# Performance work log

Measured on AMD Instinct MI355X. Metric: run time of the kernel, lower is better.

## Reference

```python
import jax, jax.numpy as jnp
import numpy as np

# Catmull-Rom basis: hermiteBasis @ tangent matrix (uniform spacing, deltas = 1,1,1)
_HERMITE = np.array([[2, -2, 1, 1], [-3, 3, -2, -1], [0, 0, 1, 0], [1, 0, 0, 0]], dtype=np.float32)
_CR = np.array([[0, 1, 0, 0], [0, 0, 1, 0], [-0.5, 0, 0.5, 0], [0, -0.5, 0, 0.5]], dtype=np.float32)
UNIFORM_BASIS = jnp.asarray(_HERMITE @ _CR)  # [[-0.5,1.5,-1.5,0.5],[1,-2.5,2,-0.5],[-0.5,0,0.5,0],[0,1,0,0]]

D, Z, Y, X, C = 16, 64, 128, 128, 2
N = 262144


def setup_inputs() -> dict:
    key = jax.random.key(0)
    k1, k2 = jax.random.split(key)
    u = jax.random.uniform(k1, (N, 3), dtype=jnp.float32)
    # zyx coords in [1, dim-3] so the 4-knot window stays mostly interior
    idx = u * jnp.array([Z - 4, Y - 4, X - 4], dtype=jnp.float32) + 1.0
    knots = jax.random.normal(k2, (D, Z, Y, X, C), dtype=jnp.float32)
    depth = jnp.float32(7.3)  # in (depths[0], depths[-1]) with depths = arange(1, D+1)
    return {"idx": idx, "knots": knots, "depth": depth}


def _spline_idx(coord, size):
    """coord: [N] float. Returns ([N,4] int knot indices, [N,4] spline weights)."""
    i0 = coord.astype(jnp.int32)                      # trunc == floor for positive coords
    s = jnp.clip(coord - i0.astype(coord.dtype), 0.0, 1.0)
    knot_idx = jnp.clip((i0 - 1)[:, None] + jnp.arange(4, dtype=jnp.int32)[None, :], 0, size - 1)
    # powers [s^3, s^2, s, 1] (explicit stack avoids 0**0 grad issues)
    powers = jnp.stack([s * s * s, s * s, s, jnp.ones_like(s)], axis=1)  # [N,4]
    return knot_idx, powers @ UNIFORM_BASIS


def reference(idx, knots, depth):
    D_, Z_, Y_, X_, _ = knots.shape
    n = idx.shape[0]
    depths = jnp.arange(1, D_ + 1, dtype=jnp.float32)  # uniform spacing -> time_diffs all 1
    ind = jnp.searchsorted(depths, depth, side='right')
    r = (depth - depths[ind - 1]) / (depths[ind] - depths[ind - 1])
    depth_coord = jnp.full((n,), (ind - 1).astype(jnp.float32) + r)

    idp, cd = _spline_idx(depth_coord, D_)
    iz, cz = _spline_idx(idx[:, 0], Z_)
    iy, cy = _spline_idx(idx[:, 1], Y_)
    ix, cx = _spline_idx(idx[:, 2], X_)

    # gather [N,4,4,4,4,C] knot neighborhood, then separable weighted reduction
    sel = knots[idp[:, :, None, None, None],
                iz[:, None, :, None, None],
                iy[:, None, None, :, None],
                ix[:, None, None, None, :]]
    return jnp.einsum('ndzyxc,nd,nz,ny,nx->nc', sel, cd, cz, cy, cx)
```

## Files before the change

### kernel.cpp

```cpp
#include <hip/hip_runtime.h>

#define Dd 16
#define Zd 64
#define Yd 128
#define Xd 128
#define Cd 2

__device__ __forceinline__ void spline_w(float coord, int size, int* idx4, float* w) {
    int i0 = (int)coord;
    float s = coord - (float)i0;
    s = fminf(fmaxf(s, 0.0f), 1.0f);
#pragma unroll
    for (int j = 0; j < 4; ++j) {
        int k = i0 - 1 + j;
        idx4[j] = min(max(k, 0), size - 1);
    }
    float s2 = s * s, s3 = s2 * s;
    w[0] = -0.5f * s3 + s2 - 0.5f * s;
    w[1] =  1.5f * s3 - 2.5f * s2 + 1.0f;
    w[2] = -1.5f * s3 + 2.0f * s2 + 0.5f * s;
    w[3] =  0.5f * s3 - 0.5f * s2;
}

__device__ __forceinline__ void depth_w(float depth, int* id4, float* wd) {
    float dc = depth - 1.0f;
    spline_w(dc, Dd, id4, wd);
}

__global__ void depth_contract_kernel(const float* __restrict__ knots,
                                      const float* __restrict__ depth_p,
                                      float4* __restrict__ Wv) {
    const int nv = Zd * Yd * Xd * Cd / 4;
    int t = blockIdx.x * blockDim.x + threadIdx.x;
    if (t >= nv) return;

    int id[4]; float wd[4];
    depth_w(depth_p[0], id, wd);

    const float4* kv = (const float4*)knots;
    const size_t slice = (size_t)Zd * Yd * Xd * Cd / 4;
    float4 a = kv[(size_t)id[0] * slice + t];
    float4 b = kv[(size_t)id[1] * slice + t];
    float4 c = kv[(size_t)id[2] * slice + t];
    float4 d = kv[(size_t)id[3] * slice + t];
    float4 r;
    r.x = wd[0] * a.x + wd[1] * b.x + wd[2] * c.x + wd[3] * d.x;
    r.y = wd[0] * a.y + wd[1] * b.y + wd[2] * c.y + wd[3] * d.y;
    r.z = wd[0] * a.z + wd[1] * b.z + wd[2] * c.z + wd[3] * d.z;
    r.w = wd[0] * a.w + wd[1] * b.w + wd[2] * c.w + wd[3] * d.w;
    Wv[t] = r;
}

__global__ void gather_eval_kernel(const float* __restrict__ idx,
                                   const float* __restrict__ W,
                                   float* __restrict__ out, int n_pts) {
    int t = blockIdx.x * blockDim.x + threadIdx.x;
    int n = t >> 2;
    int q = t & 3;
    if (n >= n_pts) return;

    float zc = idx[n * 3 + 0];
    float yc = idx[n * 3 + 1];
    float xc = idx[n * 3 + 2];

    int iz[4], iy[4], ix[4];
    float wz[4], wy[4], wx[4];
    spline_w(zc, Zd, iz, wz);
    spline_w(yc, Yd, iy, wy);
    spline_w(xc, Xd, ix, wx);

    const int ixq = ix[q];
    const float wxq = wx[q];

    const float2* __restrict__ Wv = (const float2*)W;

    float r0 = 0.0f, r1 = 0.0f;
#pragma unroll
    for (int a = 0; a < 4; ++a) {
        const int zoff = iz[a] * (Yd * Xd);
#pragma unroll
        for (int b = 0; b < 4; ++b) {
            float2 v = Wv[(size_t)(zoff + iy[b] * Xd + ixq)];
            float wzy = wz[a] * wy[b];
            r0 = fmaf(wzy, v.x, r0);
            r1 = fmaf(wzy, v.y, r1);
        }
    }
    r0 *= wxq;
    r1 *= wxq;

    r0 += __shfl_xor(r0, 1);
    r0 += __shfl_xor(r0, 2);
    r1 += __shfl_xor(r1, 1);
    r1 += __shfl_xor(r1, 2);

    if (q == 0) {
        float2* ov = (float2*)out;
        float2 o; o.x = r0; o.y = r1;
        ov[n] = o;
    }
}

__global__ void fused_kernel(const float* __restrict__ idx,
                             const float* __restrict__ knots,
                             const float* __restrict__ depth_p,
                             float* __restrict__ out, int n_pts) {
    int n = blockIdx.x * blockDim.x + threadIdx.x;
    if (n >= n_pts) return;

    int id[4]; float wd[4];
    depth_w(depth_p[0], id, wd);

    float zc = idx[n * 3 + 0];
    float yc = idx[n * 3 + 1];
    float xc = idx[n * 3 + 2];

    int iz[4], iy[4], ix[4];
    float wz[4], wy[4], wx[4];
    spline_w(zc, Zd, iz, wz);
    spline_w(yc, Yd, iy, wy);
    spline_w(xc, Xd, ix, wx);

    float acc0 = 0.0f, acc1 = 0.0f;
    for (int dd = 0; dd < 4; ++dd) {
        const float* base = knots + (size_t)id[dd] * Zd * Yd * Xd * Cd;
        float d0 = 0.0f, d1 = 0.0f;
#pragma unroll
        for (int a = 0; a < 4; ++a) {
#pragma unroll
            for (int b = 0; b < 4; ++b) {
                const float2* row = (const float2*)(base + ((size_t)(iz[a] * Yd + iy[b]) * Xd) * Cd);
                float r0 = 0.0f, r1 = 0.0f;
#pragma unroll
                for (int qq = 0; qq < 4; ++qq) {
                    float2 v = row[ix[qq]];
                    r0 = fmaf(wx[qq], v.x, r0);
                    r1 = fmaf(wx[qq], v.y, r1);
                }
                float wzy = wz[a] * wy[b];
                d0 = fmaf(wzy, r0, d0);
                d1 = fmaf(wzy, r1, d1);
            }
        }
        acc0 = fmaf(wd[dd], d0, acc0);
        acc1 = fmaf(wd[dd], d1, acc1);
    }
    out[n * 2 + 0] = acc0;
    out[n * 2 + 1] = acc1;
}

extern "C" void kernel_launch(void* const* d_in, const int* in_sizes, int n_in,
                              void* d_out, int out_size, void* d_ws, size_t ws_size,
                              hipStream_t stream) {
    const float* idx   = (const float*)d_in[0];
    const float* knots = (const float*)d_in[1];
    const float* depth = (const float*)d_in[2];
    float* out = (float*)d_out;
    const int n_pts = in_sizes[0] / 3;

    const size_t need = (size_t)Zd * Yd * Xd * Cd * sizeof(float);
    if (ws_size >= need) {
        float* W = (float*)d_ws;
        const int nv = Zd * Yd * Xd * Cd / 4;
        depth_contract_kernel<<<(nv + 255) / 256, 256, 0, stream>>>(knots, depth, (float4*)W);
        const int nthreads = n_pts * 4;
        gather_eval_kernel<<<(nthreads + 255) / 256, 256, 0, stream>>>(idx, W, out, n_pts);
    } else {
        fused_kernel<<<(n_pts + 255) / 256, 256, 0, stream>>>(idx, knots, depth, out, n_pts);
    }
}
```

Measured before the change: 213.9 us.

## Bucket-sort points by z/y tile and evaluate from LDS-resident slabs

```diff
diff --git a/kernel.cpp b/kernel.cpp
--- a/kernel.cpp
+++ b/kernel.cpp
@@ -6,6 +6,16 @@
 #define Xd 128
 #define Cd 2
 
+#define NBUCK_Z 31
+#define NBUCK_Y 16
+#define NBUCK (NBUCK_Z * NBUCK_Y)
+#define NBUCK_PAD 512
+
+#define SZ 5
+#define SY 11
+#define XPAD2 134
+#define SLAB_F4 (SZ * SY * 67)
+
 __device__ __forceinline__ void spline_w(float coord, int size, int* idx4, float* w) {
     int i0 = (int)coord;
     float s = coord - (float)i0;
@@ -22,20 +32,24 @@
     w[3] =  0.5f * s3 - 0.5f * s2;
 }
 
-__device__ __forceinline__ void depth_w(float depth, int* id4, float* wd) {
-    float dc = depth - 1.0f;
-    spline_w(dc, Dd, id4, wd);
+__device__ __forceinline__ int bucket_of(float zc, float yc) {
+    int i0z = (int)zc, i0y = (int)yc;
+    int tz = min(max(i0z >> 1, 0), NBUCK_Z - 1);
+    int ty = min(max(i0y >> 3, 0), NBUCK_Y - 1);
+    return tz * NBUCK_Y + ty;
 }
 
 __global__ void depth_contract_kernel(const float* __restrict__ knots,
                                       const float* __restrict__ depth_p,
-                                      float4* __restrict__ Wv) {
+                                      float4* __restrict__ Wv,
+                                      int* __restrict__ counts) {
     const int nv = Zd * Yd * Xd * Cd / 4;
     int t = blockIdx.x * blockDim.x + threadIdx.x;
+    if (t < NBUCK_PAD) counts[t] = 0;
     if (t >= nv) return;
 
     int id[4]; float wd[4];
-    depth_w(depth_p[0], id, wd);
+    spline_w(depth_p[0] - 1.0f, Dd, id, wd);
 
     const float4* kv = (const float4*)knots;
     const size_t slice = (size_t)Zd * Yd * Xd * Cd / 4;
@@ -51,54 +65,133 @@
     Wv[t] = r;
 }
 
+__global__ void hist_kernel(const float* __restrict__ idx, int n_pts,
+                            int* __restrict__ counts) {
+    int n = blockIdx.x * blockDim.x + threadIdx.x;
+    if (n >= n_pts) return;
+    atomicAdd(&counts[bucket_of(idx[n * 3], idx[n * 3 + 1])], 1);
+}
+
+__global__ __launch_bounds__(NBUCK_PAD) void scan_kernel(const int* __restrict__ counts,
+                                                         int* __restrict__ offsets,
+                                                         int* __restrict__ cursors) {
+    __shared__ int tmp[NBUCK_PAD];
+    int t = threadIdx.x;
+    int v = counts[t];
+    tmp[t] = v;
+    __syncthreads();
+    for (int off = 1; off < NBUCK_PAD; off <<= 1) {
+        int x = (t >= off) ? tmp[t - off] : 0;
+        __syncthreads();
+        tmp[t] += x;
+        __syncthreads();
+    }
+    int excl = tmp[t] - v;
+    offsets[t] = excl;
+    cursors[t] = excl;
+}
+
+__global__ void scatter_kernel(const float* __restrict__ idx, int n_pts,
+                               int* __restrict__ cursors,
+                               float4* __restrict__ sorted_pts) {
+    int n = blockIdx.x * blockDim.x + threadIdx.x;
+    if (n >= n_pts) return;
+    float zc = idx[n * 3], yc = idx[n * 3 + 1], xc = idx[n * 3 + 2];
+    int pos = atomicAdd(&cursors[bucket_of(zc, yc)], 1);
+    float4 sp;
+    sp.x = zc; sp.y = yc; sp.z = xc; sp.w = __int_as_float(n);
+    sorted_pts[pos] = sp;
+}
+
+__global__ __launch_bounds__(256) void bucket_eval_kernel(const float4* __restrict__ sorted_pts,
+                                                          const int* __restrict__ offsets,
+                                                          const int* __restrict__ counts,
+                                                          const float* __restrict__ W,
+                                                          float* __restrict__ out) {
+    __shared__ float4 slab4[SLAB_F4];
+    const int b = blockIdx.x;
+    const int tz = b / NBUCK_Y, ty = b - tz * NBUCK_Y;
+    const int zbase = min(max(2 * tz - 1, 0), Zd - SZ);
+    const int ybase = min(max(8 * ty - 1, 0), Yd - SY);
+    const int tid = threadIdx.x;
+
+    const float4* Wv4 = (const float4*)W;
+    for (int i = tid; i < SZ * SY * 64; i += 256) {
+        int r = i >> 6, j = i & 63;
+        int dz = r / SY, dy = r - dz * SY;
+        slab4[r * 67 + j] = Wv4[(size_t)((zbase + dz) * Yd + (ybase + dy)) * 64 + j];
+    }
+    __syncthreads();
+
+    const float2* __restrict__ slab2 = (const float2*)slab4;
+    const int start = offsets[b];
+    const int cnt4 = counts[b] * 4;
+    float2* __restrict__ ov = (float2*)out;
+
+    for (int i = tid; i < cnt4; i += 256) {
+        int p = i >> 2, q = i & 3;
+        float4 sp = sorted_pts[start + p];
+
+        int iz[4], iy[4], ix[4];
+        float wz[4], wy[4], wx[4];
+        spline_w(sp.x, Zd, iz, wz);
+        spline_w(sp.y, Yd, iy, wy);
+        spline_w(sp.z, Xd, ix, wx);
+
+        const int ixq = ix[q];
+        const float wxq = wx[q];
+
+        float r0 = 0.0f, r1 = 0.0f;
+#pragma unroll
+        for (int a = 0; a < 4; ++a) {
+            const int rz = (iz[a] - zbase) * SY;
+#pragma unroll
+            for (int bb = 0; bb < 4; ++bb) {
+                float2 v = slab2[(rz + (iy[bb] - ybase)) * XPAD2 + ixq];
+                float wzy = wz[a] * wy[bb];
+                r0 = fmaf(wzy, v.x, r0);
+                r1 = fmaf(wzy, v.y, r1);
+            }
+        }
+        r0 *= wxq; r1 *= wxq;
+        r0 += __shfl_xor(r0, 1); r0 += __shfl_xor(r0, 2);
+        r1 += __shfl_xor(r1, 1); r1 += __shfl_xor(r1, 2);
+        if (q == 0) {
+            float2 o; o.x = r0; o.y = r1;
+            ov[__float_as_int(sp.w)] = o;
+        }
+    }
+}
+
 __global__ void gather_eval_kernel(const float* __restrict__ idx,
                                    const float* __restrict__ W,
                                    float* __restrict__ out, int n_pts) {
     int t = blockIdx.x * blockDim.x + threadIdx.x;
-    int n = t >> 2;
-    int q = t & 3;
-    if (n >= n_pts) return;
-
-    float zc = idx[n * 3 + 0];
-    float yc = idx[n * 3 + 1];
-    float xc = idx[n * 3 + 2];
-
+    int n = t >> 2, q = t & 3;
+    if (n >= n_pts) return;
     int iz[4], iy[4], ix[4];
     float wz[4], wy[4], wx[4];
-    spline_w(zc, Zd, iz, wz);
-    spline_w(yc, Yd, iy, wy);
-    spline_w(xc, Xd, ix, wx);
-
-    const int ixq = ix[q];
-    const float wxq = wx[q];
-
-    const float2* __restrict__ Wv = (const float2*)W;
-
+    spline_w(idx[n * 3 + 0], Zd, iz, wz);
+    spline_w(idx[n * 3 + 1], Yd, iy, wy);
+    spline_w(idx[n * 3 + 2], Xd, ix, wx);
+    const int ixq = ix[q]; const float wxq = wx[q];
+    const float2* Wv = (const float2*)W;
     float r0 = 0.0f, r1 = 0.0f;
 #pragma unroll
     for (int a = 0; a < 4; ++a) {
         const int zoff = iz[a] * (Yd * Xd);
 #pragma unroll
-        for (int b = 0; b < 4; ++b) {
-            float2 v = Wv[(size_t)(zoff + iy[b] * Xd + ixq)];
-            float wzy = wz[a] * wy[b];
+        for (int bb = 0; bb < 4; ++bb) {
+            float2 v = Wv[(size_t)(zoff + iy[bb] * Xd + ixq)];
+            float wzy = wz[a] * wy[bb];
             r0 = fmaf(wzy, v.x, r0);
             r1 = fmaf(wzy, v.y, r1);
         }
     }
-    r0 *= wxq;
-    r1 *= wxq;
-
-    r0 += __shfl_xor(r0, 1);
-    r0 += __shfl_xor(r0, 2);
-    r1 += __shfl_xor(r1, 1);
-    r1 += __shfl_xor(r1, 2);
-
-    if (q == 0) {
-        float2* ov = (float2*)out;
-        float2 o; o.x = r0; o.y = r1;
-        ov[n] = o;
-    }
+    r0 *= wxq; r1 *= wxq;
+    r0 += __shfl_xor(r0, 1); r0 += __shfl_xor(r0, 2);
+    r1 += __shfl_xor(r1, 1); r1 += __shfl_xor(r1, 2);
+    if (q == 0) { float2 o; o.x = r0; o.y = r1; ((float2*)out)[n] = o; }
 }
 
 __global__ void fused_kernel(const float* __restrict__ idx,
@@ -107,41 +200,30 @@
                              float* __restrict__ out, int n_pts) {
     int n = blockIdx.x * blockDim.x + threadIdx.x;
     if (n >= n_pts) return;
-
     int id[4]; float wd[4];
-    depth_w(depth_p[0], id, wd);
-
-    float zc = idx[n * 3 + 0];
-    float yc = idx[n * 3 + 1];
-    float xc = idx[n * 3 + 2];
-
+    spline_w(depth_p[0] - 1.0f, Dd, id, wd);
     int iz[4], iy[4], ix[4];
     float wz[4], wy[4], wx[4];
-    spline_w(zc, Zd, iz, wz);
-    spline_w(yc, Yd, iy, wy);
-    spline_w(xc, Xd, ix, wx);
-
+    spline_w(idx[n * 3 + 0], Zd, iz, wz);
+    spline_w(idx[n * 3 + 1], Yd, iy, wy);
+    spline_w(idx[n * 3 + 2], Xd, ix, wx);
     float acc0 = 0.0f, acc1 = 0.0f;
     for (int dd = 0; dd < 4; ++dd) {
         const float* base = knots + (size_t)id[dd] * Zd * Yd * Xd * Cd;
         float d0 = 0.0f, d1 = 0.0f;
-#pragma unroll
-        for (int a = 0; a < 4; ++a) {
-#pragma unroll
-            for (int b = 0; b < 4; ++b) {
-                const float2* row = (const float2*)(base + ((size_t)(iz[a] * Yd + iy[b]) * Xd) * Cd);
+        for (int a = 0; a < 4; ++a)
+            for (int bb = 0; bb < 4; ++bb) {
+                const float2* row = (const float2*)(base + ((size_t)(iz[a] * Yd + iy[bb]) * Xd) * Cd);
                 float r0 = 0.0f, r1 = 0.0f;
-#pragma unroll
                 for (int qq = 0; qq < 4; ++qq) {
                     float2 v = row[ix[qq]];
                     r0 = fmaf(wx[qq], v.x, r0);
                     r1 = fmaf(wx[qq], v.y, r1);
                 }
-                float wzy = wz[a] * wy[b];
+                float wzy = wz[a] * wy[bb];
                 d0 = fmaf(wzy, r0, d0);
                 d1 = fmaf(wzy, r1, d1);
             }
-        }
         acc0 = fmaf(wd[dd], d0, acc0);
         acc1 = fmaf(wd[dd], d1, acc1);
     }
@@ -158,13 +240,33 @@
     float* out = (float*)d_out;
     const int n_pts = in_sizes[0] / 3;
 
-    const size_t need = (size_t)Zd * Yd * Xd * Cd * sizeof(float);
+    const size_t wBytes = (size_t)Zd * Yd * Xd * Cd * sizeof(float);
+    const size_t offCounts  = wBytes;
+    const size_t offOffsets = offCounts + NBUCK_PAD * sizeof(int);
+    const size_t offCursors = offOffsets + NBUCK_PAD * sizeof(int);
+    size_t offSorted = offCursors + NBUCK_PAD * sizeof(int);
+    offSorted = (offSorted + 15) & ~(size_t)15;
+    const size_t need = offSorted + (size_t)n_pts * sizeof(float4);
+
+    char* ws = (char*)d_ws;
+    const int nv = Zd * Yd * Xd * Cd / 4;
+
     if (ws_size >= need) {
-        float* W = (float*)d_ws;
-        const int nv = Zd * Yd * Xd * Cd / 4;
-        depth_contract_kernel<<<(nv + 255) / 256, 256, 0, stream>>>(knots, depth, (float4*)W);
-        const int nthreads = n_pts * 4;
-        gather_eval_kernel<<<(nthreads + 255) / 256, 256, 0, stream>>>(idx, W, out, n_pts);
+        float* W = (float*)(ws);
+        int* counts  = (int*)(ws + offCounts);
+        int* offsets = (int*)(ws + offOffsets);
+        int* cursors = (int*)(ws + offCursors);
+        float4* sorted_pts = (float4*)(ws + offSorted);
+
+        depth_contract_kernel<<<(nv + 255) / 256, 256, 0, stream>>>(knots, depth, (float4*)W, counts);
+        hist_kernel<<<(n_pts + 255) / 256, 256, 0, stream>>>(idx, n_pts, counts);
+        scan_kernel<<<1, NBUCK_PAD, 0, stream>>>(counts, offsets, cursors);
+        scatter_kernel<<<(n_pts + 255) / 256, 256, 0, stream>>>(idx, n_pts, cursors, sorted_pts);
+        bucket_eval_kernel<<<NBUCK, 256, 0, stream>>>(sorted_pts, offsets, counts, W, out);
+    } else if (ws_size >= wBytes) {
+        float* W = (float*)ws;
+        depth_contract_kernel<<<(nv + 255) / 256, 256, 0, stream>>>(knots, depth, (float4*)W, (int*)ws );
+        gather_eval_kernel<<<(n_pts * 4 + 255) / 256, 256, 0, stream>>>(idx, W, out, n_pts);
     } else {
         fused_kernel<<<(n_pts + 255) / 256, 256, 0, stream>>>(idx, knots, depth, out, n_pts);
     }
```

Measured after the change: 357.6 us. +67.2%, slower.
